# Performance work log

Measured on AMD Instinct MI355X. Metric: run time of the kernel, lower is better.

Reference implementation:

```python
import jax, jax.numpy as jnp
import numpy as np


def setup_inputs() -> dict:
    key = jax.random.key(0)
    k1, k2, k3, k4 = jax.random.split(key, 4)
    B, L, T = 8, 2048, 1024
    Dh, Dg, Dp = 1024, 768, 256
    H = jax.random.normal(k1, (B, L, Dh), dtype=jnp.float32)
    G = jax.random.normal(k2, (B, T, Dg), dtype=jnp.float32)
    # nn.Linear(d_g, d_proj, bias=False).weight -> [d_proj, d_g]
    Wq = jax.random.normal(k3, (Dp, Dg), dtype=jnp.float32) * (Dg ** -0.5)
    Wk = jax.random.normal(k4, (Dp, Dh), dtype=jnp.float32) * (Dh ** -0.5)
    return {"H": H, "G": G, "Wq": Wq, "Wk": Wk}


def reference(H, G, Wq, Wk):
    # GO-token queries attend over protein residues; values are the raw H.
    # The torch module computes this with streaming chunks + online LSE,
    # which is mathematically identical to a single stable softmax attention.
    d_proj = Wq.shape[0]
    scale = d_proj ** -0.5
    Q = jnp.einsum('btg,pg->btp', G, Wq)          # [B,T,Dp]
    K = jnp.einsum('blh,ph->blp', H, Wk)          # [B,L,Dp]
    logits = jnp.einsum('btp,blp->btl', Q, K) * scale  # [B,T,L] fp32
    alpha = jax.nn.softmax(logits, axis=-1)
    # denominator clamp matches torch's s.clamp_min(1e-20) (no-op for unmasked)
    Z = jnp.einsum('btl,blh->bth', alpha, H)      # [B,T,Dh]
    return Z
```

## Files before the change

### kernel.cpp

```cpp
#include <hip/hip_runtime.h>
#include <hip/hip_bf16.h>
#include <type_traits>


typedef float    f32x4  __attribute__((ext_vector_type(4)));
typedef __bf16   bf16x8 __attribute__((ext_vector_type(8)));
typedef unsigned short u16x8 __attribute__((ext_vector_type(8)));

__device__ __forceinline__ unsigned short f2bf(float f) {
    union { float f; unsigned u; } x; x.f = f;
    return (unsigned short)((x.u + 0x7fffu + ((x.u >> 16) & 1u)) >> 16);
}
__device__ __forceinline__ float bf2f(unsigned short u) {
    union { unsigned u; float f; } x; x.u = ((unsigned)u) << 16;
    return x.f;
}
__device__ __forceinline__ void gload_lds16(const unsigned short* g, unsigned short* l) {
    __builtin_amdgcn_global_load_lds(
        (const __attribute__((address_space(1))) void*)g,
        (__attribute__((address_space(3))) void*)l, 16, 0, 0);
}

__global__ __launch_bounds__(256) void kn_transp(const float* __restrict__ H,
                                                 unsigned short* __restrict__ HT,
                                                 int L, int D) {
    __shared__ float tile[32][33];
    int b = blockIdx.z;
    const float* src = H + (size_t)b * L * D;
    unsigned short* dstT = HT + (size_t)b * L * D;
    int l0 = blockIdx.y * 32, d0 = blockIdx.x * 32;
    int tx = threadIdx.x, ty = threadIdx.y;
#pragma unroll
    for (int i = ty; i < 32; i += 8)
        tile[i][tx] = src[(size_t)(l0 + i) * D + d0 + tx];
    __syncthreads();
#pragma unroll
    for (int i = ty; i < 32; i += 8)
        dstT[(size_t)(d0 + i) * L + l0 + tx] = f2bf(tile[tx][i]);
}

template<int TM, int WM>
__device__ __forceinline__ void proj_body(const float* __restrict__ A,
                                          const float* __restrict__ B,
                                          unsigned short* __restrict__ C,
                                          int N, int K, int gxs) {
    constexpr int WN  = 4 / WM;
    constexpr int MF  = (TM / WM) / 16;
    constexpr int NF  = (128 / WN) / 16;
    constexpr int CHA = TM * 8;
    constexpr int CHT = CHA + 1024;
    constexpr int CPT = CHT / 256;
    constexpr int BUFU = TM * 64 + 128 * 64;
    constexpr int LDSB = (2 * BUFU * 2 > TM * 132 * 4) ? 2 * BUFU * 2 : TM * 132 * 4;
    __shared__ __align__(16) char smem_raw[LDSB];
    unsigned short* base = (unsigned short*)smem_raw;
    float* st = (float*)smem_raw;

    int tid = threadIdx.x;
    int t = blockIdx.x;
    int by = t >> gxs;
    int bx = t & ((1 << gxs) - 1);
    const float* Ab = A + (size_t)by * TM * K;
    const float* Bb = B + (size_t)bx * 128 * K;

    int lane = tid & 63;
    int wid = tid >> 6;
    int wr = wid / WN, wc = wid % WN;
    int lr = lane & 15;
    int lg = lane >> 4;
    int xoff = (lane & 7) << 3;

    f32x4 rv[CPT][2];
    f32x4 acc[MF][NF] = {};

    auto LOAD = [&](int k0) {
#pragma unroll
        for (int c = 0; c < CPT; ++c) {
            int ch = c * 256 + tid;
            const float* src;
            if (ch < CHA) {
                int row = ch >> 3;
                src = Ab + (size_t)row * K + k0 + (ch & 7) * 8;
            } else {
                int bc = ch - CHA;
                int row = bc >> 3;
                src = Bb + (size_t)row * K + k0 + (bc & 7) * 8;
            }
            rv[c][0] = *(const f32x4*)src;
            rv[c][1] = *(const f32x4*)(src + 4);
        }
    };
    auto WRITE = [&](int buf) {
        unsigned short* dA = base + buf * BUFU;
        unsigned short* dB = dA + TM * 64;
#pragma unroll
        for (int c = 0; c < CPT; ++c) {
            int ch = c * 256 + tid;
            u16x8 o;
#pragma unroll
            for (int j = 0; j < 4; ++j) { o[j] = f2bf(rv[c][0][j]); o[4 + j] = f2bf(rv[c][1][j]); }
            if (ch < CHA) {
                int row = ch >> 3;
                int sl = (ch & 7) ^ (row & 7);
                *(u16x8*)&dA[row * 64 + sl * 8] = o;
            } else {
                int bc = ch - CHA;
                int row = bc >> 3;
                int sl = (bc & 7) ^ (row & 7);
                *(u16x8*)&dB[row * 64 + sl * 8] = o;
            }
        }
    };
    auto COMPUTE = [&](int buf) {
        unsigned short* pA = base + buf * BUFU;
        unsigned short* pB = pA + TM * 64;
#pragma unroll
        for (int kk = 0; kk < 2; ++kk) {
            int kb = (kk * 32 + lg * 8) ^ xoff;
            bf16x8 af[MF], bfr[NF];
#pragma unroll
            for (int m = 0; m < MF; ++m)
                af[m] = *(const bf16x8*)&pA[(wr * MF * 16 + m * 16 + lr) * 64 + kb];
#pragma unroll
            for (int n = 0; n < NF; ++n)
                bfr[n] = *(const bf16x8*)&pB[(wc * NF * 16 + n * 16 + lr) * 64 + kb];
#pragma unroll
            for (int m = 0; m < MF; ++m)
#pragma unroll
                for (int n = 0; n < NF; ++n)
                    acc[m][n] = __builtin_amdgcn_mfma_f32_16x16x32_bf16(af[m], bfr[n], acc[m][n], 0, 0, 0);
        }
    };

    int nt = K / 64;
    LOAD(0);
    WRITE(0);
    __syncthreads();
    int buf = 0;
    for (int tt = 0; tt < nt; ++tt) {
        if (tt + 1 < nt) LOAD((tt + 1) * 64);
        COMPUTE(buf);
        if (tt + 1 < nt) WRITE(buf ^ 1);
        __syncthreads();
        buf ^= 1;
    }

#pragma unroll
    for (int m = 0; m < MF; ++m) {
        int r0 = wr * MF * 16 + m * 16 + lg * 4;
#pragma unroll
        for (int n = 0; n < NF; ++n) {
            int c0 = wc * NF * 16 + n * 16 + lr;
#pragma unroll
            for (int j = 0; j < 4; ++j)
                st[(r0 + j) * 132 + c0] = acc[m][n][j];
        }
    }
    __syncthreads();
    constexpr int TPR = 256 / TM;
    constexpr int CW  = 128 / TPR;
    int r  = tid / TPR;
    int c0 = (tid % TPR) * CW;
    size_t grow = (size_t)(by * TM + r) * N + bx * 128 + c0;
#pragma unroll
    for (int g = 0; g < CW / 8; ++g) {
        f32x4 a = *(const f32x4*)&st[r * 132 + c0 + g * 8];
        f32x4 b = *(const f32x4*)&st[r * 132 + c0 + g * 8 + 4];
        u16x8 o;
#pragma unroll
        for (int j = 0; j < 4; ++j) { o[j] = f2bf(a[j]); o[4 + j] = f2bf(b[j]); }
        *(u16x8*)&C[grow + g * 8] = o;
    }
}

__global__ __launch_bounds__(256) void kn_qproj(const float* A, const float* B,
                                                unsigned short* C, int N, int K, int gxs) {
    proj_body<32, 1>(A, B, C, N, K, gxs);
}
__global__ __launch_bounds__(256) void kn_kproj(const float* A, const float* B,
                                                unsigned short* C, int N, int K, int gxs) {
    proj_body<64, 2>(A, B, C, N, K, gxs);
}

__global__ __launch_bounds__(512) void kn_sgemm(const unsigned short* __restrict__ A,
                                                const unsigned short* __restrict__ B,
                                                unsigned short* __restrict__ C,
                                                float* __restrict__ rowsum,
                                                int N, int K, int Trows,
                                                long batchA, long batchB, long batchC,
                                                float scale, int gxs) {
    __shared__ __align__(16) char smem_raw[49152];
    unsigned short* base = (unsigned short*)smem_raw;
    float* st = (float*)smem_raw;

    int tid = threadIdx.x;
    int wg = blockIdx.x;
    int bz = wg & 7;
    int t = wg >> 3;
    int by = t >> gxs;
    int bx = t & ((1 << gxs) - 1);

    const unsigned short* Ab = A + (size_t)bz * batchA + (size_t)by * 256 * K;
    const unsigned short* Bb = B + (size_t)bz * batchB + (size_t)bx * 128 * K;
    unsigned short* Cb = C + (size_t)bz * batchC;
    float* rs = rowsum + (size_t)bz * Trows;

    int lane = tid & 63;
    int wid = tid >> 6;
    int wr = wid >> 1, wc = wid & 1;
    int lr = lane & 15;
    int lg = lane >> 4;
    int xoff = (lane & 7) << 3;

    f32x4 acc[4][4] = {};

    for (int k0 = 0; k0 < K; k0 += 64) {
#pragma unroll
        for (int c = 0; c < 6; ++c) {
            int ch = c * 512 + tid;
            if (ch < 2048) {
                int row = ch >> 3;
                int g8 = (ch & 7) ^ (row & 7);
                gload_lds16(Ab + (size_t)row * K + k0 + g8 * 8, base + ch * 8);
            } else {
                int bc = ch - 2048;
                int row = bc >> 3;
                int g8 = (bc & 7) ^ (row & 7);
                gload_lds16(Bb + (size_t)row * K + k0 + g8 * 8, base + 16384 + bc * 8);
            }
        }
        __syncthreads();
#pragma unroll
        for (int kk = 0; kk < 2; ++kk) {
            int kb = (kk * 32 + lg * 8) ^ xoff;
            bf16x8 af[4], bfr[4];
#pragma unroll
            for (int m = 0; m < 4; ++m)
                af[m] = *(const bf16x8*)&base[(wr * 64 + m * 16 + lr) * 64 + kb];
#pragma unroll
            for (int n = 0; n < 4; ++n)
                bfr[n] = *(const bf16x8*)&base[16384 + (wc * 64 + n * 16 + lr) * 64 + kb];
#pragma unroll
            for (int m = 0; m < 4; ++m)
#pragma unroll
                for (int n = 0; n < 4; ++n)
                    acc[m][n] = __builtin_amdgcn_mfma_f32_16x16x32_bf16(af[m], bfr[n], acc[m][n], 0, 0, 0);
        }
        __syncthreads();
    }

#pragma unroll
    for (int q = 0; q < 4; ++q) {
        if (wr == q) {
#pragma unroll
            for (int m = 0; m < 4; ++m) {
                int rl = m * 16 + lg * 4;
#pragma unroll
                for (int n = 0; n < 4; ++n) {
                    int col = wc * 64 + n * 16 + lr;
#pragma unroll
                    for (int j = 0; j < 4; ++j)
                        st[(rl + j) * 132 + col] = acc[m][n][j] * scale;
                }
            }
        }
        __syncthreads();
        int r = tid >> 3;
        int c0 = (tid & 7) * 16;
        size_t grow = (size_t)(by * 256 + q * 64 + r) * N + bx * 128 + c0;
        float psum = 0.f;
#pragma unroll
        for (int g = 0; g < 2; ++g) {
            f32x4 a = *(const f32x4*)&st[r * 132 + c0 + g * 8];
            f32x4 b = *(const f32x4*)&st[r * 132 + c0 + g * 8 + 4];
            u16x8 o;
#pragma unroll
            for (int j = 0; j < 4; ++j) {
                float pa = __expf(a[j]);
                float pb = __expf(b[j]);
                o[j] = f2bf(pa); o[4 + j] = f2bf(pb);
                psum += bf2f(o[j]) + bf2f(o[4 + j]);
            }
            *(u16x8*)&Cb[grow + g * 8] = o;
        }
        psum += __shfl_xor(psum, 1);
        psum += __shfl_xor(psum, 2);
        psum += __shfl_xor(psum, 4);
        if ((tid & 7) == 0)
            atomicAdd(&rs[by * 256 + q * 64 + r], psum);
        __syncthreads();
    }
}

__global__ __launch_bounds__(512) void kn_pv(const unsigned short* __restrict__ A,
                                             const unsigned short* __restrict__ B,
                                             float* __restrict__ C,
                                             const float* __restrict__ rowsum,
                                             int N, int K, int Trows,
                                             long batchA, long batchB, long batchC,
                                             int gxs) {
    __shared__ __align__(16) char smem_raw[3 * 49152];
    unsigned short* base = (unsigned short*)smem_raw;
    float* st = (float*)smem_raw;

    int tid = threadIdx.x;
    int wg = blockIdx.x;
    int bz = wg & 7;
    int t = wg >> 3;
    int by = t >> gxs;
    int bx = t & ((1 << gxs) - 1);

    const unsigned short* Ab = A + (size_t)bz * batchA + (size_t)by * 256 * K;
    const unsigned short* Bb = B + (size_t)bz * batchB + (size_t)bx * 128 * K;
    float* Cb = C + (size_t)bz * batchC;
    const float* rs = rowsum + (size_t)bz * Trows;

    int lane = tid & 63;
    int wid = tid >> 6;
    int wr = wid >> 1, wc = wid & 1;
    int lr = lane & 15;
    int lg = lane >> 4;
    int xoff = (lane & 7) << 3;

    f32x4 acc[4][4] = {};
    bf16x8 fA0[4], fB0[4], fA1[4], fB1[4];

    auto STAGE_HALF = [&](int buf, int k0, int half) {
        unsigned short* dA = base + buf * 24576;
        unsigned short* dB = dA + 16384;
#pragma unroll
        for (int c = 0; c < 3; ++c) {
            int ch = half * 1536 + c * 512 + tid;
            if (ch < 2048) {
                int row = ch >> 3;
                int g8 = (ch & 7) ^ (row & 7);
                gload_lds16(Ab + (size_t)row * K + k0 + g8 * 8, dA + ch * 8);
            } else {
                int bc = ch - 2048;
                int row = bc >> 3;
                int g8 = (bc & 7) ^ (row & 7);
                gload_lds16(Bb + (size_t)row * K + k0 + g8 * 8, dB + bc * 8);
            }
        }
    };
    auto LDFRAG = [&](int buf, int kk, bf16x8* fa, bf16x8* fb) {
        unsigned short* pA = base + buf * 24576;
        unsigned short* pB = pA + 16384;
        int kb = (kk * 32 + lg * 8) ^ xoff;
#pragma unroll
        for (int m = 0; m < 4; ++m)
            fa[m] = *(const bf16x8*)&pA[(wr * 64 + m * 16 + lr) * 64 + kb];
#pragma unroll
        for (int n = 0; n < 4; ++n)
            fb[n] = *(const bf16x8*)&pB[(wc * 64 + n * 16 + lr) * 64 + kb];
    };

    int nt = K / 64;
    STAGE_HALF(0, 0, 0);   STAGE_HALF(0, 0, 1);
    STAGE_HALF(1, 64, 0);  STAGE_HALF(1, 64, 1);
    asm volatile("s_waitcnt vmcnt(6)" ::: "memory");
    __builtin_amdgcn_s_barrier();
    LDFRAG(0, 0, fA0, fB0);

    int cur = 0;
    for (int tt = 0; tt < nt; ++tt) {
        int nb  = (cur >= 1) ? cur - 1 : 2;
        int nxt = (cur == 2) ? 0 : cur + 1;
        if (tt + 2 < nt) STAGE_HALF(nb, (tt + 2) * 64, 0);
        LDFRAG(cur, 1, fA1, fB1);
        __builtin_amdgcn_sched_barrier(0);
        __builtin_amdgcn_s_setprio(1);
#pragma unroll
        for (int m = 0; m < 4; ++m)
#pragma unroll
            for (int n = 0; n < 4; ++n)
                acc[m][n] = __builtin_amdgcn_mfma_f32_16x16x32_bf16(fA0[m], fB0[n], acc[m][n], 0, 0, 0);
        __builtin_amdgcn_s_setprio(0);
        __builtin_amdgcn_sched_barrier(0);
        if (tt + 2 < nt) STAGE_HALF(nb, (tt + 2) * 64, 1);
        __builtin_amdgcn_sched_barrier(0);
        __builtin_amdgcn_s_setprio(1);
#pragma unroll
        for (int m = 0; m < 4; ++m)
#pragma unroll
            for (int n = 0; n < 4; ++n)
                acc[m][n] = __builtin_amdgcn_mfma_f32_16x16x32_bf16(fA1[m], fB1[n], acc[m][n], 0, 0, 0);
        __builtin_amdgcn_s_setprio(0);
        __builtin_amdgcn_sched_barrier(0);
        if (tt + 1 < nt) {
            if (tt + 2 < nt) asm volatile("s_waitcnt vmcnt(6)" ::: "memory");
            else             asm volatile("s_waitcnt vmcnt(0)" ::: "memory");
            LDFRAG(nxt, 0, fA0, fB0);
            __builtin_amdgcn_sched_barrier(0);
            __builtin_amdgcn_s_barrier();
        }
        cur = nxt;
    }
    __syncthreads();

#pragma unroll
    for (int q = 0; q < 4; ++q) {
        if (wr == q) {
#pragma unroll
            for (int m = 0; m < 4; ++m) {
                int rl = m * 16 + lg * 4;
#pragma unroll
                for (int n = 0; n < 4; ++n) {
                    int col = wc * 64 + n * 16 + lr;
#pragma unroll
                    for (int j = 0; j < 4; ++j)
                        st[(rl + j) * 132 + col] = acc[m][n][j];
                }
            }
        }
        __syncthreads();
        int r = tid >> 3;
        int c0 = (tid & 7) * 16;
        float inv = 1.0f / rs[by * 256 + q * 64 + r];
        size_t grow = (size_t)(by * 256 + q * 64 + r) * N + bx * 128 + c0;
#pragma unroll
        for (int g = 0; g < 4; ++g) {
            f32x4 v = *(const f32x4*)&st[r * 132 + c0 + g * 4];
#pragma unroll
            for (int j = 0; j < 4; ++j) v[j] *= inv;
            *(f32x4*)&Cb[grow + g * 4] = v;
        }
        __syncthreads();
    }
}

extern "C" void kernel_launch(void* const* d_in, const int* in_sizes, int n_in,
                              void* d_out, int out_size, void* d_ws, size_t ws_size,
                              hipStream_t stream) {
    constexpr int B = 8, L = 2048, T = 1024, Dh = 1024, Dg = 768, Dp = 256;
    const float* H  = (const float*)d_in[0];
    const float* G  = (const float*)d_in[1];
    const float* Wq = (const float*)d_in[2];
    const float* Wk = (const float*)d_in[3];
    float* Z = (float*)d_out;

    unsigned short* Qbf = (unsigned short*)d_ws;
    unsigned short* Kbf = Qbf + (size_t)B * T * Dp;
    unsigned short* HT  = Kbf + (size_t)B * L * Dp;
    unsigned short* S   = HT  + (size_t)B * Dh * L;
    float* rowsum = (float*)(S + (size_t)B * T * L);

    hipMemsetAsync(rowsum, 0, (size_t)B * T * sizeof(float), stream);

    kn_transp<<<dim3(Dh / 32, L / 32, B), dim3(32, 8), 0, stream>>>(H, HT, L, Dh);

    kn_qproj<<<(B * T / 32) * (Dp / 128), 256, 0, stream>>>(G, Wq, Qbf, Dp, Dg, 1);

    kn_kproj<<<(B * L / 64) * (Dp / 128), 256, 0, stream>>>(H, Wk, Kbf, Dp, Dh, 1);

    kn_sgemm<<<(T / 256) * (L / 128) * B, 512, 0, stream>>>
        (Qbf, Kbf, S, rowsum, L, Dp, T, (long)T * Dp, (long)L * Dp, (long)T * L, 0.0625f, 4);

    kn_pv<<<(T / 256) * (Dh / 128) * B, 512, 0, stream>>>
        (S, HT, Z, rowsum, Dh, L, T, (long)T * L, (long)Dh * L, (long)T * Dh, 3);
}
```

Baseline: 147.5 us.

## Prefetch full K into LDS with staged waits in sgemm, retile to 128 rows

The QK^T logits GEMM now issues all four K-slices of A and B into LDS at the start, then waits on them stage by stage using vmcnt counters. This replaces the per-iteration load-then-sync loop and overlaps the remaining loads with MFMA work. The tile height drops from 256 to 128 rows, doubling the number of workgroups. The transpose kernel also moves from 32x32 to 64x64 tiles. Costs: 128KB of LDS per block limits occupancy to one block per CU, and K is hard-coded to 256.

```diff
diff --git a/kernel.cpp b/kernel.cpp
--- a/kernel.cpp
+++ b/kernel.cpp
@@ -24,18 +24,18 @@
 __global__ __launch_bounds__(256) void kn_transp(const float* __restrict__ H,
                                                  unsigned short* __restrict__ HT,
                                                  int L, int D) {
-    __shared__ float tile[32][33];
+    __shared__ float tile[64][65];
     int b = blockIdx.z;
     const float* src = H + (size_t)b * L * D;
     unsigned short* dstT = HT + (size_t)b * L * D;
-    int l0 = blockIdx.y * 32, d0 = blockIdx.x * 32;
+    int l0 = blockIdx.y * 64, d0 = blockIdx.x * 64;
     int tx = threadIdx.x, ty = threadIdx.y;
 #pragma unroll
-    for (int i = ty; i < 32; i += 8)
+    for (int i = ty; i < 64; i += 4)
         tile[i][tx] = src[(size_t)(l0 + i) * D + d0 + tx];
     __syncthreads();
 #pragma unroll
-    for (int i = ty; i < 32; i += 8)
+    for (int i = ty; i < 64; i += 4)
         dstT[(size_t)(d0 + i) * L + l0 + tx] = f2bf(tile[tx][i]);
 }
 
@@ -186,12 +186,14 @@
                                                 const unsigned short* __restrict__ B,
                                                 unsigned short* __restrict__ C,
                                                 float* __restrict__ rowsum,
-                                                int N, int K, int Trows,
+                                                int N, int Trows,
                                                 long batchA, long batchB, long batchC,
                                                 float scale, int gxs) {
-    __shared__ __align__(16) char smem_raw[49152];
-    unsigned short* base = (unsigned short*)smem_raw;
-    float* st = (float*)smem_raw;
+    constexpr int K = 256;
+    __shared__ __align__(16) unsigned short sm[128 * 256 * 2];
+    unsigned short* sA = sm;
+    unsigned short* sB = sm + 128 * 256;
+    float* st = (float*)sm;
 
     int tid = threadIdx.x;
     int wg = blockIdx.x;
@@ -200,7 +202,7 @@
     int by = t >> gxs;
     int bx = t & ((1 << gxs) - 1);
 
-    const unsigned short* Ab = A + (size_t)bz * batchA + (size_t)by * 256 * K;
+    const unsigned short* Ab = A + (size_t)bz * batchA + (size_t)by * 128 * K;
     const unsigned short* Bb = B + (size_t)bz * batchB + (size_t)bx * 128 * K;
     unsigned short* Cb = C + (size_t)bz * batchC;
     float* rs = rowsum + (size_t)bz * Trows;
@@ -212,48 +214,58 @@
     int lg = lane >> 4;
     int xoff = (lane & 7) << 3;
 
-    f32x4 acc[4][4] = {};
-
-    for (int k0 = 0; k0 < K; k0 += 64) {
-#pragma unroll
-        for (int c = 0; c < 6; ++c) {
+#pragma unroll
+    for (int p = 0; p < 4; ++p) {
+#pragma unroll
+        for (int c = 0; c < 2; ++c) {
             int ch = c * 512 + tid;
-            if (ch < 2048) {
-                int row = ch >> 3;
-                int g8 = (ch & 7) ^ (row & 7);
-                gload_lds16(Ab + (size_t)row * K + k0 + g8 * 8, base + ch * 8);
-            } else {
-                int bc = ch - 2048;
-                int row = bc >> 3;
-                int g8 = (bc & 7) ^ (row & 7);
-                gload_lds16(Bb + (size_t)row * K + k0 + g8 * 8, base + 16384 + bc * 8);
-            }
-        }
-        __syncthreads();
+            int row = ch >> 3;
+            int g8 = (ch & 7) ^ (row & 7);
+            gload_lds16(Ab + (size_t)row * K + p * 64 + g8 * 8, sA + p * 8192 + ch * 8);
+        }
+#pragma unroll
+        for (int c = 0; c < 2; ++c) {
+            int ch = c * 512 + tid;
+            int row = ch >> 3;
+            int g8 = (ch & 7) ^ (row & 7);
+            gload_lds16(Bb + (size_t)row * K + p * 64 + g8 * 8, sB + p * 8192 + ch * 8);
+        }
+    }
+
+    f32x4 acc[2][4] = {};
+#pragma unroll
+    for (int p = 0; p < 4; ++p) {
+        if (p == 0)      asm volatile("s_waitcnt vmcnt(12)" ::: "memory");
+        else if (p == 1) asm volatile("s_waitcnt vmcnt(8)" ::: "memory");
+        else if (p == 2) asm volatile("s_waitcnt vmcnt(4)" ::: "memory");
+        else             asm volatile("s_waitcnt vmcnt(0)" ::: "memory");
+        __builtin_amdgcn_s_barrier();
+        unsigned short* pA = sA + p * 8192;
+        unsigned short* pB = sB + p * 8192;
 #pragma unroll
         for (int kk = 0; kk < 2; ++kk) {
             int kb = (kk * 32 + lg * 8) ^ xoff;
-            bf16x8 af[4], bfr[4];
-#pragma unroll
-            for (int m = 0; m < 4; ++m)
-                af[m] = *(const bf16x8*)&base[(wr * 64 + m * 16 + lr) * 64 + kb];
+            bf16x8 af[2], bfr[4];
+#pragma unroll
+            for (int m = 0; m < 2; ++m)
+                af[m] = *(const bf16x8*)&pA[(wr * 32 + m * 16 + lr) * 64 + kb];
 #pragma unroll
             for (int n = 0; n < 4; ++n)
-                bfr[n] = *(const bf16x8*)&base[16384 + (wc * 64 + n * 16 + lr) * 64 + kb];
-#pragma unroll
-            for (int m = 0; m < 4; ++m)
+                bfr[n] = *(const bf16x8*)&pB[(wc * 64 + n * 16 + lr) * 64 + kb];
+#pragma unroll
+            for (int m = 0; m < 2; ++m)
 #pragma unroll
                 for (int n = 0; n < 4; ++n)
                     acc[m][n] = __builtin_amdgcn_mfma_f32_16x16x32_bf16(af[m], bfr[n], acc[m][n], 0, 0, 0);
         }
-        __syncthreads();
-    }
+    }
+    __syncthreads();
 
 #pragma unroll
     for (int q = 0; q < 4; ++q) {
         if (wr == q) {
 #pragma unroll
-            for (int m = 0; m < 4; ++m) {
+            for (int m = 0; m < 2; ++m) {
                 int rl = m * 16 + lg * 4;
 #pragma unroll
                 for (int n = 0; n < 4; ++n) {
@@ -265,29 +277,27 @@
             }
         }
         __syncthreads();
-        int r = tid >> 3;
-        int c0 = (tid & 7) * 16;
-        size_t grow = (size_t)(by * 256 + q * 64 + r) * N + bx * 128 + c0;
+        int r  = tid >> 4;
+        int c0 = (tid & 15) * 8;
+        int grow_r = by * 128 + q * 32 + r;
+        size_t grow = (size_t)grow_r * N + bx * 128 + c0;
+        f32x4 a = *(const f32x4*)&st[r * 132 + c0];
+        f32x4 b = *(const f32x4*)&st[r * 132 + c0 + 4];
+        u16x8 o;
         float psum = 0.f;
 #pragma unroll
-        for (int g = 0; g < 2; ++g) {
-            f32x4 a = *(const f32x4*)&st[r * 132 + c0 + g * 8];
-            f32x4 b = *(const f32x4*)&st[r * 132 + c0 + g * 8 + 4];
-            u16x8 o;
-#pragma unroll
-            for (int j = 0; j < 4; ++j) {
-                float pa = __expf(a[j]);
-                float pb = __expf(b[j]);
-                o[j] = f2bf(pa); o[4 + j] = f2bf(pb);
-                psum += bf2f(o[j]) + bf2f(o[4 + j]);
-            }
-            *(u16x8*)&Cb[grow + g * 8] = o;
-        }
+        for (int j = 0; j < 4; ++j) {
+            o[j]     = f2bf(__expf(a[j]));
+            o[4 + j] = f2bf(__expf(b[j]));
+            psum += bf2f(o[j]) + bf2f(o[4 + j]);
+        }
+        *(u16x8*)&Cb[grow] = o;
         psum += __shfl_xor(psum, 1);
         psum += __shfl_xor(psum, 2);
         psum += __shfl_xor(psum, 4);
-        if ((tid & 7) == 0)
-            atomicAdd(&rs[by * 256 + q * 64 + r], psum);
+        psum += __shfl_xor(psum, 8);
+        if ((tid & 15) == 0)
+            atomicAdd(&rs[grow_r], psum);
         __syncthreads();
     }
 }
@@ -447,14 +457,14 @@
 
     hipMemsetAsync(rowsum, 0, (size_t)B * T * sizeof(float), stream);
 
-    kn_transp<<<dim3(Dh / 32, L / 32, B), dim3(32, 8), 0, stream>>>(H, HT, L, Dh);
+    kn_transp<<<dim3(Dh / 64, L / 64, B), dim3(64, 4), 0, stream>>>(H, HT, L, Dh);
 
     kn_qproj<<<(B * T / 32) * (Dp / 128), 256, 0, stream>>>(G, Wq, Qbf, Dp, Dg, 1);
 
     kn_kproj<<<(B * L / 64) * (Dp / 128), 256, 0, stream>>>(H, Wk, Kbf, Dp, Dh, 1);
 
-    kn_sgemm<<<(T / 256) * (L / 128) * B, 512, 0, stream>>>
-        (Qbf, Kbf, S, rowsum, L, Dp, T, (long)T * Dp, (long)L * Dp, (long)T * L, 0.0625f, 4);
+    kn_sgemm<<<(T / 128) * (L / 128) * B, 512, 0, stream>>>
+        (Qbf, Kbf, S, rowsum, L, T, (long)T * Dp, (long)L * Dp, (long)T * L, 0.0625f, 4);
 
     kn_pv<<<(T / 256) * (Dh / 128) * B, 512, 0, stream>>>
         (S, HT, Z, rowsum, Dh, L, T, (long)T * L, (long)Dh * L, (long)T * Dh, 3);
```

Measured after the change: 149.5 us. About the same (+1.3%).

## Emit bf16 copy of H in transpose kernel and feed K-projection from it

Applied to the files above, without the earlier changes.

The transpose kernel now also writes a row-major bf16 copy of H, using larger 64x64 tiles. The K-projection then reads that bf16 copy straight into LDS with global_load_lds instead of re-reading fp32 H and converting it. This halves the bytes the K-projection reads for H, but adds a 32MB write in the transpose and drops the double buffering in kproj. f2bf now uses the compiler's native bf16 conversion.

```diff
diff --git a/kernel.cpp b/kernel.cpp
--- a/kernel.cpp
+++ b/kernel.cpp
@@ -8,8 +8,9 @@
 typedef unsigned short u16x8 __attribute__((ext_vector_type(8)));
 
 __device__ __forceinline__ unsigned short f2bf(float f) {
-    union { float f; unsigned u; } x; x.f = f;
-    return (unsigned short)((x.u + 0x7fffu + ((x.u >> 16) & 1u)) >> 16);
+    union { __bf16 b; unsigned short u; } c;
+    c.b = (__bf16)f;
+    return c.u;
 }
 __device__ __forceinline__ float bf2f(unsigned short u) {
     union { unsigned u; float f; } x; x.u = ((unsigned)u) << 16;
@@ -23,36 +24,37 @@
 
 __global__ __launch_bounds__(256) void kn_transp(const float* __restrict__ H,
                                                  unsigned short* __restrict__ HT,
+                                                 unsigned short* __restrict__ Hbf,
                                                  int L, int D) {
-    __shared__ float tile[32][33];
+    __shared__ float tile[64][65];
     int b = blockIdx.z;
     const float* src = H + (size_t)b * L * D;
     unsigned short* dstT = HT + (size_t)b * L * D;
-    int l0 = blockIdx.y * 32, d0 = blockIdx.x * 32;
+    unsigned short* dstN = Hbf + (size_t)b * L * D;
+    int l0 = blockIdx.y * 64, d0 = blockIdx.x * 64;
     int tx = threadIdx.x, ty = threadIdx.y;
 #pragma unroll
-    for (int i = ty; i < 32; i += 8)
-        tile[i][tx] = src[(size_t)(l0 + i) * D + d0 + tx];
+    for (int i = ty; i < 64; i += 4) {
+        float v = src[(size_t)(l0 + i) * D + d0 + tx];
+        tile[i][tx] = v;
+        dstN[(size_t)(l0 + i) * D + d0 + tx] = f2bf(v);
+    }
     __syncthreads();
 #pragma unroll
-    for (int i = ty; i < 32; i += 8)
+    for (int i = ty; i < 64; i += 4)
         dstT[(size_t)(d0 + i) * L + l0 + tx] = f2bf(tile[tx][i]);
 }
 
-template<int TM, int WM>
-__device__ __forceinline__ void proj_body(const float* __restrict__ A,
-                                          const float* __restrict__ B,
-                                          unsigned short* __restrict__ C,
-                                          int N, int K, int gxs) {
-    constexpr int WN  = 4 / WM;
-    constexpr int MF  = (TM / WM) / 16;
-    constexpr int NF  = (128 / WN) / 16;
+__global__ __launch_bounds__(256) void kn_qproj(const float* __restrict__ A,
+                                                const float* __restrict__ B,
+                                                unsigned short* __restrict__ C,
+                                                int N, int K, int gxs) {
+    constexpr int TM = 32;
+    constexpr int MF = 2, NF = 2;
     constexpr int CHA = TM * 8;
-    constexpr int CHT = CHA + 1024;
-    constexpr int CPT = CHT / 256;
+    constexpr int CPT = (CHA + 1024) / 256;
     constexpr int BUFU = TM * 64 + 128 * 64;
-    constexpr int LDSB = (2 * BUFU * 2 > TM * 132 * 4) ? 2 * BUFU * 2 : TM * 132 * 4;
-    __shared__ __align__(16) char smem_raw[LDSB];
+    __shared__ __align__(16) char smem_raw[2 * BUFU * 2 > TM * 132 * 4 ? 2 * BUFU * 2 : TM * 132 * 4];
     unsigned short* base = (unsigned short*)smem_raw;
     float* st = (float*)smem_raw;
 
@@ -65,7 +67,6 @@
 
     int lane = tid & 63;
     int wid = tid >> 6;
-    int wr = wid / WN, wc = wid % WN;
     int lr = lane & 15;
     int lg = lane >> 4;
     int xoff = (lane & 7) << 3;
@@ -78,14 +79,8 @@
         for (int c = 0; c < CPT; ++c) {
             int ch = c * 256 + tid;
             const float* src;
-            if (ch < CHA) {
-                int row = ch >> 3;
-                src = Ab + (size_t)row * K + k0 + (ch & 7) * 8;
-            } else {
-                int bc = ch - CHA;
-                int row = bc >> 3;
-                src = Bb + (size_t)row * K + k0 + (bc & 7) * 8;
-            }
+            if (ch < CHA) { int row = ch >> 3; src = Ab + (size_t)row * K + k0 + (ch & 7) * 8; }
+            else { int bc = ch - CHA; int row = bc >> 3; src = Bb + (size_t)row * K + k0 + (bc & 7) * 8; }
             rv[c][0] = *(const f32x4*)src;
             rv[c][1] = *(const f32x4*)(src + 4);
         }
@@ -100,13 +95,10 @@
 #pragma unroll
             for (int j = 0; j < 4; ++j) { o[j] = f2bf(rv[c][0][j]); o[4 + j] = f2bf(rv[c][1][j]); }
             if (ch < CHA) {
-                int row = ch >> 3;
-                int sl = (ch & 7) ^ (row & 7);
+                int row = ch >> 3; int sl = (ch & 7) ^ (row & 7);
                 *(u16x8*)&dA[row * 64 + sl * 8] = o;
             } else {
-                int bc = ch - CHA;
-                int row = bc >> 3;
-                int sl = (bc & 7) ^ (row & 7);
+                int bc = ch - CHA; int row = bc >> 3; int sl = (bc & 7) ^ (row & 7);
                 *(u16x8*)&dB[row * 64 + sl * 8] = o;
             }
         }
@@ -120,10 +112,10 @@
             bf16x8 af[MF], bfr[NF];
 #pragma unroll
             for (int m = 0; m < MF; ++m)
-                af[m] = *(const bf16x8*)&pA[(wr * MF * 16 + m * 16 + lr) * 64 + kb];
+                af[m] = *(const bf16x8*)&pA[(m * 16 + lr) * 64 + kb];
 #pragma unroll
             for (int n = 0; n < NF; ++n)
-                bfr[n] = *(const bf16x8*)&pB[(wc * NF * 16 + n * 16 + lr) * 64 + kb];
+                bfr[n] = *(const bf16x8*)&pB[(wid * 32 + n * 16 + lr) * 64 + kb];
 #pragma unroll
             for (int m = 0; m < MF; ++m)
 #pragma unroll
@@ -133,8 +125,7 @@
     };
 
     int nt = K / 64;
-    LOAD(0);
-    WRITE(0);
+    LOAD(0); WRITE(0);
     __syncthreads();
     int buf = 0;
     for (int tt = 0; tt < nt; ++tt) {
@@ -147,23 +138,21 @@
 
 #pragma unroll
     for (int m = 0; m < MF; ++m) {
-        int r0 = wr * MF * 16 + m * 16 + lg * 4;
+        int r0 = m * 16 + lg * 4;
 #pragma unroll
         for (int n = 0; n < NF; ++n) {
-            int c0 = wc * NF * 16 + n * 16 + lr;
+            int c0 = wid * 32 + n * 16 + lr;
 #pragma unroll
             for (int j = 0; j < 4; ++j)
                 st[(r0 + j) * 132 + c0] = acc[m][n][j];
         }
     }
     __syncthreads();
-    constexpr int TPR = 256 / TM;
-    constexpr int CW  = 128 / TPR;
-    int r  = tid / TPR;
-    int c0 = (tid % TPR) * CW;
+    int r  = tid >> 3;
+    int c0 = (tid & 7) * 16;
     size_t grow = (size_t)(by * TM + r) * N + bx * 128 + c0;
 #pragma unroll
-    for (int g = 0; g < CW / 8; ++g) {
+    for (int g = 0; g < 2; ++g) {
         f32x4 a = *(const f32x4*)&st[r * 132 + c0 + g * 8];
         f32x4 b = *(const f32x4*)&st[r * 132 + c0 + g * 8 + 4];
         u16x8 o;
@@ -173,13 +162,96 @@
     }
 }
 
-__global__ __launch_bounds__(256) void kn_qproj(const float* A, const float* B,
-                                                unsigned short* C, int N, int K, int gxs) {
-    proj_body<32, 1>(A, B, C, N, K, gxs);
-}
-__global__ __launch_bounds__(256) void kn_kproj(const float* A, const float* B,
-                                                unsigned short* C, int N, int K, int gxs) {
-    proj_body<64, 2>(A, B, C, N, K, gxs);
+__global__ __launch_bounds__(256) void kn_kproj(const unsigned short* __restrict__ A,
+                                                const float* __restrict__ B,
+                                                unsigned short* __restrict__ C,
+                                                int N, int K, int gxs) {
+    __shared__ __align__(16) char smem_raw[64 * 132 * 4];
+    unsigned short* sA = (unsigned short*)smem_raw;
+    unsigned short* sB = sA + 64 * 64;
+    float* st = (float*)smem_raw;
+
+    int tid = threadIdx.x;
+    int t = blockIdx.x;
+    int by = t >> gxs;
+    int bx = t & ((1 << gxs) - 1);
+    const unsigned short* Ab = A + (size_t)by * 64 * K;
+    const float* Bb = B + (size_t)bx * 128 * K;
+
+    int lane = tid & 63;
+    int wid = tid >> 6;
+    int wr = wid >> 1, wc = wid & 1;
+    int lr = lane & 15;
+    int lg = lane >> 4;
+    int xoff = (lane & 7) << 3;
+
+    f32x4 acc[2][4] = {};
+
+    for (int k0 = 0; k0 < K; k0 += 64) {
+#pragma unroll
+        for (int c = 0; c < 2; ++c) {
+            int ch = c * 256 + tid;
+            int row = ch >> 3;
+            int g8 = (ch & 7) ^ (row & 7);
+            gload_lds16(Ab + (size_t)row * K + k0 + g8 * 8, sA + ch * 8);
+        }
+#pragma unroll
+        for (int c = 0; c < 4; ++c) {
+            int ch = c * 256 + tid;
+            int row = ch >> 3;
+            const float* src = Bb + (size_t)row * K + k0 + (ch & 7) * 8;
+            f32x4 v0 = *(const f32x4*)src;
+            f32x4 v1 = *(const f32x4*)(src + 4);
+            u16x8 o;
+#pragma unroll
+            for (int j = 0; j < 4; ++j) { o[j] = f2bf(v0[j]); o[4 + j] = f2bf(v1[j]); }
+            int sl = (ch & 7) ^ (row & 7);
+            *(u16x8*)&sB[row * 64 + sl * 8] = o;
+        }
+        __syncthreads();
+#pragma unroll
+        for (int kk = 0; kk < 2; ++kk) {
+            int kb = (kk * 32 + lg * 8) ^ xoff;
+            bf16x8 af[2], bfr[4];
+#pragma unroll
+            for (int m = 0; m < 2; ++m)
+                af[m] = *(const bf16x8*)&sA[(wr * 32 + m * 16 + lr) * 64 + kb];
+#pragma unroll
+            for (int n = 0; n < 4; ++n)
+                bfr[n] = *(const bf16x8*)&sB[(wc * 64 + n * 16 + lr) * 64 + kb];
+#pragma unroll
+            for (int m = 0; m < 2; ++m)
+#pragma unroll
+                for (int n = 0; n < 4; ++n)
+                    acc[m][n] = __builtin_amdgcn_mfma_f32_16x16x32_bf16(af[m], bfr[n], acc[m][n], 0, 0, 0);
+        }
+        __syncthreads();
+    }
+
+#pragma unroll
+    for (int m = 0; m < 2; ++m) {
+        int r0 = wr * 32 + m * 16 + lg * 4;
+#pragma unroll
+        for (int n = 0; n < 4; ++n) {
+            int c0 = wc * 64 + n * 16 + lr;
+#pragma unroll
+            for (int j = 0; j < 4; ++j)
+                st[(r0 + j) * 132 + c0] = acc[m][n][j];
+        }
+    }
+    __syncthreads();
+    int r  = tid >> 2;
+    int c0 = (tid & 3) * 32;
+    size_t grow = (size_t)(by * 64 + r) * N + bx * 128 + c0;
+#pragma unroll
+    for (int g = 0; g < 4; ++g) {
+        f32x4 a = *(const f32x4*)&st[r * 132 + c0 + g * 8];
+        f32x4 b = *(const f32x4*)&st[r * 132 + c0 + g * 8 + 4];
+        u16x8 o;
+#pragma unroll
+        for (int j = 0; j < 4; ++j) { o[j] = f2bf(a[j]); o[4 + j] = f2bf(b[j]); }
+        *(u16x8*)&C[grow + g * 8] = o;
+    }
 }
 
 __global__ __launch_bounds__(512) void kn_sgemm(const unsigned short* __restrict__ A,
@@ -267,7 +339,8 @@
         __syncthreads();
         int r = tid >> 3;
         int c0 = (tid & 7) * 16;
-        size_t grow = (size_t)(by * 256 + q * 64 + r) * N + bx * 128 + c0;
+        int grow_r = by * 256 + q * 64 + r;
+        size_t grow = (size_t)grow_r * N + bx * 128 + c0;
         float psum = 0.f;
 #pragma unroll
         for (int g = 0; g < 2; ++g) {
@@ -276,9 +349,8 @@
             u16x8 o;
 #pragma unroll
             for (int j = 0; j < 4; ++j) {
-                float pa = __expf(a[j]);
-                float pb = __expf(b[j]);
-                o[j] = f2bf(pa); o[4 + j] = f2bf(pb);
+                o[j]     = f2bf(__expf(a[j]));
+                o[4 + j] = f2bf(__expf(b[j]));
                 psum += bf2f(o[j]) + bf2f(o[4 + j]);
             }
             *(u16x8*)&Cb[grow + g * 8] = o;
@@ -287,7 +359,7 @@
         psum += __shfl_xor(psum, 2);
         psum += __shfl_xor(psum, 4);
         if ((tid & 7) == 0)
-            atomicAdd(&rs[by * 256 + q * 64 + r], psum);
+            atomicAdd(&rs[grow_r], psum);
         __syncthreads();
     }
 }
@@ -443,15 +515,16 @@
     unsigned short* Kbf = Qbf + (size_t)B * T * Dp;
     unsigned short* HT  = Kbf + (size_t)B * L * Dp;
     unsigned short* S   = HT  + (size_t)B * Dh * L;
-    float* rowsum = (float*)(S + (size_t)B * T * L);
+    unsigned short* Hbf = S   + (size_t)B * T * L;
+    float* rowsum = (float*)(Hbf + (size_t)B * L * Dh);
 
     hipMemsetAsync(rowsum, 0, (size_t)B * T * sizeof(float), stream);
 
-    kn_transp<<<dim3(Dh / 32, L / 32, B), dim3(32, 8), 0, stream>>>(H, HT, L, Dh);
+    kn_transp<<<dim3(Dh / 64, L / 64, B), dim3(64, 4), 0, stream>>>(H, HT, Hbf, L, Dh);
 
     kn_qproj<<<(B * T / 32) * (Dp / 128), 256, 0, stream>>>(G, Wq, Qbf, Dp, Dg, 1);
 
-    kn_kproj<<<(B * L / 64) * (Dp / 128), 256, 0, stream>>>(H, Wk, Kbf, Dp, Dh, 1);
+    kn_kproj<<<(B * L / 64) * (Dp / 128), 256, 0, stream>>>(Hbf, Wk, Kbf, Dp, Dh, 1);
 
     kn_sgemm<<<(T / 256) * (L / 128) * B, 512, 0, stream>>>
         (Qbf, Kbf, S, rowsum, L, Dp, T, (long)T * Dp, (long)L * Dp, (long)T * L, 0.0625f, 4);
```

Measured after the change: 141.9 us. 3.8% less time.
